# Kernel optimization log

Measured on AMD Instinct MI355X. Metric: run time of the kernel, lower is better.

Reference implementation:

```python
import jax, jax.numpy as jnp
import numpy as np

CLASS_TOKEN_INDEX = 1
MAX_PROMPTS = 25
MAX_TEXT_LEN = 3500
THRESHOLD = 0.5
B, S, D, E = 8, 4096, 768, 128
P = E * (E - 1) // 2  # 8128 candidate span pairs


def setup_inputs() -> dict:
    rng = np.random.default_rng(0)
    input_ids = rng.integers(5, 30000, size=(B, S)).astype(np.int64)
    words_mask = np.zeros((B, S), dtype=np.int64)
    attention_mask = np.zeros((B, S), dtype=np.int64)
    text_lengths = np.zeros((B, 1), dtype=np.int64)
    for b in range(B):
        ns = int(rng.integers(10, MAX_PROMPTS + 1))  # number of entity-type prompt tokens
        input_ids[b][input_ids[b] == CLASS_TOKEN_INDEX] = 5  # remove stray specials
        input_ids[b, :ns] = CLASS_TOKEN_INDEX
        L = int(rng.integers(3000, MAX_TEXT_LEN + 1))  # number of words in text
        words_mask[b, ns:ns + L] = np.arange(1, L + 1)
        attention_mask[b, :ns + L] = 1
        text_lengths[b, 0] = L
    key = jax.random.key(0)
    k1, k2, k3 = jax.random.split(key, 3)
    return {
        "token_embeds": jax.random.normal(k1, (B, S, D), dtype=jnp.float32),
        "adj": jax.random.uniform(k2, (B, E, E), dtype=jnp.float32),
        "span_rep": jax.random.normal(k3, (B, E, D), dtype=jnp.float32),
        "input_ids": jnp.asarray(input_ids),
        "attention_mask": jnp.asarray(attention_mask),
        "text_lengths": jnp.asarray(text_lengths),
        "words_mask": jnp.asarray(words_mask),
    }


def _extract_special(token_embeds, input_ids):
    # pack embeddings at positions where input_ids == class token, left-aligned
    special = input_ids == CLASS_TOKEN_INDEX                      # (B,S)
    num_special = special.sum(-1, keepdims=True)                  # (B,1)
    slot = jnp.cumsum(special, axis=-1) - 1                       # packed slot per special
    tgt = jnp.where(special, slot, MAX_PROMPTS)                   # dump pads into extra slot
    bidx = jnp.arange(B)[:, None]
    emb = jnp.zeros((B, MAX_PROMPTS + 1, D), token_embeds.dtype)
    emb = emb.at[bidx, tgt].add(token_embeds * special[..., None].astype(token_embeds.dtype))
    emb = emb[:, :MAX_PROMPTS]
    mask = (jnp.arange(MAX_PROMPTS)[None, :] < num_special).astype(jnp.int64)
    return emb, mask


def _extract_words(token_embeds, words_mask, text_lengths):
    # scatter token embeddings into word slots: words_embedding[b, words_mask[b,j]-1] = token_embeds[b,j]
    is_word = words_mask > 0
    tgt = jnp.where(is_word, words_mask - 1, MAX_TEXT_LEN)        # dump pads into extra slot
    bidx = jnp.arange(B)[:, None]
    we = jnp.zeros((B, MAX_TEXT_LEN + 1, D), token_embeds.dtype)
    we = we.at[bidx, tgt].add(token_embeds * is_word[..., None].astype(token_embeds.dtype))
    we = we[:, :MAX_TEXT_LEN]
    mask = jnp.arange(MAX_TEXT_LEN)[None, :] < text_lengths       # (B,MAX_TEXT_LEN) bool
    return we, mask


def _build_entity_pairs(adj, span_rep):
    rows, cols = jnp.triu_indices(E, k=1)                         # (P,), (P,)
    vals = adj[:, rows, cols]                                     # (B,P)
    sel = vals > THRESHOLD
    # stable left-packing: selected pairs first, preserving triu order (matches per-batch torch loop)
    order = jnp.argsort((~sel).astype(jnp.int32), axis=1, stable=True)
    pair_mask = jnp.take_along_axis(sel, order, axis=1)           # (B,P) bool
    r = rows[order]                                               # (B,P)
    c = cols[order]
    pair_idx = jnp.where(pair_mask[..., None], jnp.stack([r, c], axis=-1), -1)
    bidx = jnp.arange(B)[:, None]
    head_rep = span_rep[bidx, jnp.where(pair_mask, r, 0)]         # pads gather span 0 (clamp_min(0))
    tail_rep = span_rep[bidx, jnp.where(pair_mask, c, 0)]
    return pair_idx, pair_mask, head_rep, tail_rep


def reference(token_embeds, adj, span_rep, input_ids, attention_mask, text_lengths, words_mask):
    prompts_embedding, prompts_embedding_mask = _extract_special(token_embeds, input_ids)
    words_embedding, word_mask = _extract_words(token_embeds, words_mask, text_lengths)
    pair_idx, pair_mask, head_rep, tail_rep = _build_entity_pairs(adj, span_rep)
    return (prompts_embedding, prompts_embedding_mask, words_embedding, word_mask,
            pair_idx, pair_mask, head_rep, tail_rep)
```

## Files before the change

kernel.cpp:

```cpp
#include <hip/hip_runtime.h>

#define BB 8
#define SS 4096
#define DD 768
#define EE 128
#define PP 8128
#define MP 25
#define MT 3500
#define D4 192
#define NROWS_W (BB*MT)
#define NROWS_P (BB*PP)
#define R_TOTAL (NROWS_W + 2*NROWS_P)

typedef float f32x4 __attribute__((ext_vector_type(4)));

__global__ __launch_bounds__(1024) void k_prep(
    const float* __restrict__ te, const int* __restrict__ ids,
    const float* __restrict__ adj, const int* __restrict__ wm,
    const int* __restrict__ tlen,
    float* __restrict__ out0, float* __restrict__ out1,
    float* __restrict__ out3, float* __restrict__ out4, float* __restrict__ out5,
    int* __restrict__ wordpos, int* __restrict__ hsrc, int* __restrict__ tsrc)
{
    int b = blockIdx.x;
    int t = threadIdx.x, wave = t >> 6, lane = t & 63;
    __shared__ int pos[MP];
    __shared__ int spos[16 * 32];
    __shared__ int wcnt[16];
    __shared__ int woff[17];
    __shared__ int wsum[16];

    if (t < MP) pos[t] = -1;

    {
        const int* row = ids + b * SS;
        int base = 0;
        for (int c = 0; c < 4; ++c) {
            int p = wave * 256 + c * 64 + lane;
            bool s = (row[p] == 1);
            unsigned long long m = __ballot(s);
            if (s) {
                int sl = base + __popcll(m & ((1ull << lane) - 1ull));
                if (sl < 32) spos[wave * 32 + sl] = p;
            }
            base += __popcll(m);
        }
        if (lane == 0) wcnt[wave] = base;
    }
    __syncthreads();
    if (t == 0) {
        int acc = 0;
        for (int w = 0; w < 16; ++w) { woff[w] = acc; acc += wcnt[w]; }
        woff[16] = acc;
    }
    __syncthreads();
    {
        int cnt = wcnt[wave]; if (cnt > 32) cnt = 32;
        if (lane < cnt) {
            int g = woff[wave] + lane;
            if (g < MP) pos[g] = spos[wave * 32 + lane];
        }
    }

    int L = tlen[b];
    for (int i = t; i < MT; i += 1024) {
        out3[b * MT + i] = (i < L) ? 1.0f : 0.0f;
        wordpos[b * MT + i] = -1;
    }
    __syncthreads();

    for (int i = t; i < SS; i += 1024) {
        int v = wm[b * SS + i];
        if (v > 0 && v <= MT) wordpos[b * MT + v - 1] = i;
    }

    int nspec = woff[16];
    if (t < MP) out1[b * MP + t] = (t < nspec) ? 1.0f : 0.0f;
    {
        const f32x4* te4 = (const f32x4*)te;
        f32x4* o4 = (f32x4*)out0;
        for (int idx = t; idx < MP * D4; idx += 1024) {
            int j = idx / D4, e = idx - j * D4;
            int src = pos[j];
            f32x4 v = (f32x4)(0.0f);
            if (src >= 0) v = te4[((size_t)(b * SS + src)) * D4 + e];
            o4[((size_t)(b * MP + j)) * D4 + e] = v;
        }
    }

    int r8[8], c8[8]; bool s8[8]; int my = 0;
    for (int i = 0; i < 8; ++i) {
        int p = t * 8 + i;
        r8[i] = 0; c8[i] = 0; s8[i] = false;
        if (p < PP) {
            int lo = 0, hi = EE - 2;
            while (lo < hi) {
                int mid = (lo + hi + 1) >> 1;
                int st = mid * (2 * EE - 1 - mid) / 2;
                if (st <= p) lo = mid; else hi = mid - 1;
            }
            int r = lo;
            int st = r * (2 * EE - 1 - r) / 2;
            int c = r + 1 + (p - st);
            r8[i] = r; c8[i] = c;
            s8[i] = adj[((size_t)b * EE + r) * EE + c] > 0.5f;
            my += s8[i] ? 1 : 0;
        }
    }
    int inc = my;
    for (int off = 1; off < 64; off <<= 1) {
        int n = __shfl_up(inc, off);
        if (lane >= off) inc += n;
    }
    if (lane == 63) wsum[wave] = inc;
    __syncthreads();
    int wv_off = 0, K = 0;
    for (int w = 0; w < 16; ++w) {
        int s = wsum[w];
        if (w < wave) wv_off += s;
        K += s;
    }
    int selb = wv_off + inc - my;
    for (int i = 0; i < 8; ++i) {
        int p = t * 8 + i;
        if (p >= PP) break;
        int q;
        if (s8[i]) { q = selb; ++selb; }
        else       { q = K + (p - selb); }
        size_t oq = (size_t)b * PP + q;
        out4[oq * 2 + 0] = s8[i] ? (float)r8[i] : -1.0f;
        out4[oq * 2 + 1] = s8[i] ? (float)c8[i] : -1.0f;
        out5[oq]         = s8[i] ? 1.0f : 0.0f;
        hsrc[oq]         = s8[i] ? r8[i] : 0;
        tsrc[oq]         = s8[i] ? c8[i] : 0;
    }
}

__global__ __launch_bounds__(256) void k_gather(
    const float* __restrict__ te, const float* __restrict__ sr,
    const int* __restrict__ wordpos, const int* __restrict__ hsrc,
    const int* __restrict__ tsrc,
    float* __restrict__ out2, float* __restrict__ out6, float* __restrict__ out7)
{
    int gw = blockIdx.x * 4 + (threadIdx.x >> 6);
    int lane = threadIdx.x & 63;
    int nw = gridDim.x * 4;
    const f32x4* te4 = (const f32x4*)te;
    const f32x4* sr4 = (const f32x4*)sr;
    for (int row = gw; row < R_TOTAL; row += nw) {
        const f32x4* src4;
        f32x4* dst4;
        bool valid = true;
        bool stream_src = false;
        if (row < NROWS_W) {
            int b = row / MT;
            int s = wordpos[row];
            valid = (s >= 0);
            src4 = te4 + ((size_t)(b * SS + s)) * D4;
            dst4 = (f32x4*)out2 + (size_t)row * D4;
            stream_src = true;
        } else {
            int idx2 = row - NROWS_W;
            bool head = idx2 < NROWS_P;
            int idx = head ? idx2 : idx2 - NROWS_P;
            int b = idx / PP;
            int s = head ? hsrc[idx] : tsrc[idx];
            src4 = sr4 + ((size_t)(b * EE + s)) * D4;
            dst4 = (f32x4*)(head ? out6 : out7) + (size_t)idx * D4;
        }
        #pragma unroll
        for (int k = 0; k < 3; ++k) {
            f32x4 v;
            if (valid) {
                v = stream_src ? __builtin_nontemporal_load(&src4[lane + 64 * k])
                               : src4[lane + 64 * k];
            } else {
                v = (f32x4)(0.0f);
            }
            __builtin_nontemporal_store(v, &dst4[lane + 64 * k]);
        }
    }
}

extern "C" void kernel_launch(void* const* d_in, const int* in_sizes, int n_in,
                              void* d_out, int out_size, void* d_ws, size_t ws_size,
                              hipStream_t stream) {
    const float* te   = (const float*)d_in[0];
    const float* adj  = (const float*)d_in[1];
    const float* sr   = (const float*)d_in[2];
    const int*   ids  = (const int*)d_in[3];
    const int*   tlen = (const int*)d_in[5];
    const int*   wm   = (const int*)d_in[6];
    float* out = (float*)d_out;

    size_t off0 = 0;
    size_t off1 = off0 + (size_t)BB * MP * DD;
    size_t off2 = off1 + (size_t)BB * MP;
    size_t off3 = off2 + (size_t)BB * MT * DD;
    size_t off4 = off3 + (size_t)BB * MT;
    size_t off5 = off4 + (size_t)BB * PP * 2;
    size_t off6 = off5 + (size_t)BB * PP;
    size_t off7 = off6 + (size_t)BB * PP * DD;

    int* wordpos = (int*)d_ws;
    int* hsrc = wordpos + BB * MT;
    int* tsrc = hsrc + BB * PP;

    k_prep<<<BB, 1024, 0, stream>>>(te, ids, adj, wm, tlen,
                                    out + off0, out + off1, out + off3,
                                    out + off4, out + off5,
                                    wordpos, hsrc, tsrc);
    k_gather<<<2048, 256, 0, stream>>>(te, sr, wordpos, hsrc, tsrc,
                                       out + off2, out + off6, out + off7);
}
```

Baseline: 160.2 us.

## Move prompt gather and pair metadata writes into gather kernel; pack pair records

The prompt-embedding copy and the pair_idx/pair_mask output writes move out of the 8-block prep kernel into the wide gather kernel. The prep kernel now writes only one packed int per pair (selection flag, row, col) plus the special-token positions to workspace. This shortens the serial, low-parallelism prep stage and spreads those stores across many waves. Gather stores also switch from nontemporal to regular stores, which may change how the large output writes behave in cache.

Result: faster. 150.4 us (-6.1%).

```diff
diff --git a/kernel.cpp b/kernel.cpp
--- a/kernel.cpp
+++ b/kernel.cpp
@@ -8,29 +8,29 @@
 #define MP 25
 #define MT 3500
 #define D4 192
-#define NROWS_W (BB*MT)
-#define NROWS_P (BB*PP)
-#define R_TOTAL (NROWS_W + 2*NROWS_P)
+#define NROWS_W  (BB*MT)
+#define NROWS_P  (BB*PP)
+#define NROWS_PR (BB*MP)
+#define R_TOTAL  (NROWS_W + 2*NROWS_P + NROWS_PR)
 
 typedef float f32x4 __attribute__((ext_vector_type(4)));
 
 __global__ __launch_bounds__(1024) void k_prep(
-    const float* __restrict__ te, const int* __restrict__ ids,
-    const float* __restrict__ adj, const int* __restrict__ wm,
-    const int* __restrict__ tlen,
-    float* __restrict__ out0, float* __restrict__ out1,
-    float* __restrict__ out3, float* __restrict__ out4, float* __restrict__ out5,
-    int* __restrict__ wordpos, int* __restrict__ hsrc, int* __restrict__ tsrc)
+    const int* __restrict__ ids, const float* __restrict__ adj,
+    const int* __restrict__ wm, const int* __restrict__ tlen,
+    float* __restrict__ out3,
+    int* __restrict__ wordpos, int* __restrict__ pairrec,
+    int* __restrict__ pos, int* __restrict__ nspec)
 {
     int b = blockIdx.x;
     int t = threadIdx.x, wave = t >> 6, lane = t & 63;
-    __shared__ int pos[MP];
+    __shared__ int pos_s[MP];
     __shared__ int spos[16 * 32];
     __shared__ int wcnt[16];
     __shared__ int woff[17];
     __shared__ int wsum[16];
 
-    if (t < MP) pos[t] = -1;
+    if (t < MP) pos_s[t] = -1;
 
     {
         const int* row = ids + b * SS;
@@ -58,7 +58,7 @@
         int cnt = wcnt[wave]; if (cnt > 32) cnt = 32;
         if (lane < cnt) {
             int g = woff[wave] + lane;
-            if (g < MP) pos[g] = spos[wave * 32 + lane];
+            if (g < MP) pos_s[g] = spos[wave * 32 + lane];
         }
     }
 
@@ -73,20 +73,8 @@
         int v = wm[b * SS + i];
         if (v > 0 && v <= MT) wordpos[b * MT + v - 1] = i;
     }
-
-    int nspec = woff[16];
-    if (t < MP) out1[b * MP + t] = (t < nspec) ? 1.0f : 0.0f;
-    {
-        const f32x4* te4 = (const f32x4*)te;
-        f32x4* o4 = (f32x4*)out0;
-        for (int idx = t; idx < MP * D4; idx += 1024) {
-            int j = idx / D4, e = idx - j * D4;
-            int src = pos[j];
-            f32x4 v = (f32x4)(0.0f);
-            if (src >= 0) v = te4[((size_t)(b * SS + src)) * D4 + e];
-            o4[((size_t)(b * MP + j)) * D4 + e] = v;
-        }
-    }
+    if (t < MP) pos[b * MP + t] = pos_s[t];
+    if (t == 0) nspec[b] = woff[16];
 
     int r8[8], c8[8]; bool s8[8]; int my = 0;
     for (int i = 0; i < 8; ++i) {
@@ -127,20 +115,18 @@
         int q;
         if (s8[i]) { q = selb; ++selb; }
         else       { q = K + (p - selb); }
-        size_t oq = (size_t)b * PP + q;
-        out4[oq * 2 + 0] = s8[i] ? (float)r8[i] : -1.0f;
-        out4[oq * 2 + 1] = s8[i] ? (float)c8[i] : -1.0f;
-        out5[oq]         = s8[i] ? 1.0f : 0.0f;
-        hsrc[oq]         = s8[i] ? r8[i] : 0;
-        tsrc[oq]         = s8[i] ? c8[i] : 0;
+        unsigned rec = s8[i] ? (0x80000000u | ((unsigned)r8[i] << 8) | (unsigned)c8[i]) : 0u;
+        pairrec[(size_t)b * PP + q] = (int)rec;
     }
 }
 
 __global__ __launch_bounds__(256) void k_gather(
     const float* __restrict__ te, const float* __restrict__ sr,
-    const int* __restrict__ wordpos, const int* __restrict__ hsrc,
-    const int* __restrict__ tsrc,
-    float* __restrict__ out2, float* __restrict__ out6, float* __restrict__ out7)
+    const int* __restrict__ wordpos, const int* __restrict__ pairrec,
+    const int* __restrict__ pos, const int* __restrict__ nspec,
+    float* __restrict__ out0, float* __restrict__ out1, float* __restrict__ out2,
+    float* __restrict__ out4, float* __restrict__ out5,
+    float* __restrict__ out6, float* __restrict__ out7)
 {
     int gw = blockIdx.x * 4 + (threadIdx.x >> 6);
     int lane = threadIdx.x & 63;
@@ -159,25 +145,42 @@
             src4 = te4 + ((size_t)(b * SS + s)) * D4;
             dst4 = (f32x4*)out2 + (size_t)row * D4;
             stream_src = true;
-        } else {
+        } else if (row < NROWS_W + 2 * NROWS_P) {
             int idx2 = row - NROWS_W;
             bool head = idx2 < NROWS_P;
             int idx = head ? idx2 : idx2 - NROWS_P;
             int b = idx / PP;
-            int s = head ? hsrc[idx] : tsrc[idx];
+            unsigned rec = (unsigned)pairrec[idx];
+            int r = (rec >> 8) & 0x7F;
+            int c = rec & 0xFF;
+            int s = head ? r : c;
             src4 = sr4 + ((size_t)(b * EE + s)) * D4;
             dst4 = (f32x4*)(head ? out6 : out7) + (size_t)idx * D4;
+            if (head && lane == 0) {
+                bool sel = rec != 0u;
+                out4[(size_t)idx * 2 + 0] = sel ? (float)r : -1.0f;
+                out4[(size_t)idx * 2 + 1] = sel ? (float)c : -1.0f;
+                out5[idx] = sel ? 1.0f : 0.0f;
+            }
+        } else {
+            int j2 = row - (NROWS_W + 2 * NROWS_P);
+            int b = j2 / MP;
+            int j = j2 - b * MP;
+            int s = pos[j2];
+            valid = (s >= 0);
+            src4 = te4 + ((size_t)(b * SS + s)) * D4;
+            dst4 = (f32x4*)out0 + (size_t)j2 * D4;
+            stream_src = true;
+            if (lane == 0) out1[j2] = (j < nspec[b]) ? 1.0f : 0.0f;
         }
         #pragma unroll
         for (int k = 0; k < 3; ++k) {
-            f32x4 v;
+            f32x4 v = (f32x4)(0.0f);
             if (valid) {
                 v = stream_src ? __builtin_nontemporal_load(&src4[lane + 64 * k])
                                : src4[lane + 64 * k];
-            } else {
-                v = (f32x4)(0.0f);
-            }
-            __builtin_nontemporal_store(v, &dst4[lane + 64 * k]);
+            }
+            dst4[lane + 64 * k] = v;
         }
     }
 }
@@ -203,13 +206,14 @@
     size_t off7 = off6 + (size_t)BB * PP * DD;
 
     int* wordpos = (int*)d_ws;
-    int* hsrc = wordpos + BB * MT;
-    int* tsrc = hsrc + BB * PP;
-
-    k_prep<<<BB, 1024, 0, stream>>>(te, ids, adj, wm, tlen,
-                                    out + off0, out + off1, out + off3,
-                                    out + off4, out + off5,
-                                    wordpos, hsrc, tsrc);
-    k_gather<<<2048, 256, 0, stream>>>(te, sr, wordpos, hsrc, tsrc,
-                                       out + off2, out + off6, out + off7);
+    int* pairrec = wordpos + BB * MT;
+    int* pos     = pairrec + BB * PP;
+    int* nspec   = pos + BB * MP;
+
+    k_prep<<<BB, 1024, 0, stream>>>(ids, adj, wm, tlen, out + off3,
+                                    wordpos, pairrec, pos, nspec);
+    k_gather<<<2048, 256, 0, stream>>>(te, sr, wordpos, pairrec, pos, nspec,
+                                       out + off0, out + off1, out + off2,
+                                       out + off4, out + off5,
+                                       out + off6, out + off7);
 }
```
